# Kernel tuning notes

Measured on AMD Instinct MI355X. Metric: run time of the kernel, lower is better.

The kernel has to match this reference:

```python
import jax, jax.numpy as jnp
import numpy as np

B, N, D = 2, 2048, 1024          # batch, seq (= wh*ww), model dim
H, HD = 16, 64                   # heads, head_dim (inner_dim = H*HD = D)
MLP = 4096                       # SwiGLU hidden dim
WSY, WSX = 16, 32                # ws_y = wh//2, ws_x = ww//2  (wh=32, ww=64)
EPS = float(jnp.finfo(jnp.float32).eps)  # torch RMSNorm default eps


def setup_inputs() -> dict:
    key = jax.random.key(0)
    ks = jax.random.split(key, 8)
    return {
        "x": jax.random.normal(ks[0], (B, N, D), jnp.float32),
        "t": jax.random.normal(ks[1], (B,), jnp.float32),
        "dt": jax.random.normal(ks[2], (B, D), jnp.float32),
        "w_qkv": (jax.random.normal(ks[3], (3 * H * HD, D), jnp.float32) * 0.02),
        "w_o": (jax.random.normal(ks[4], (D, H * HD), jnp.float32) * 0.02),
        "w1": (jax.random.normal(ks[5], (2 * MLP, D), jnp.float32) * 0.02),
        "w2": (jax.random.normal(ks[6], (D, MLP), jnp.float32) * 0.02),
        "g_attn": jnp.ones((D,), jnp.float32),  # RMSNorm weight (attn)
        "g_ff": jnp.ones((D,), jnp.float32),    # RMSNorm weight (ffn)
    }


def _rms(x, g):
    return x * jax.lax.rsqrt(jnp.mean(x * x, axis=-1, keepdims=True) + EPS) * g


def _win(x):
    # 'b h (wc_y wc_x ws_y ws_x) d' -> 'b h (wc_y ws_y wc_x ws_x) d'
    b, h, n, d = x.shape
    return x.reshape(b, h, 2, 2, WSY, WSX, d).transpose(0, 1, 2, 4, 3, 5, 6).reshape(b, h, n, d)


def _unwin(x):
    # inverse of _win
    b, h, n, d = x.shape
    return x.reshape(b, h, 2, WSY, 2, WSX, d).transpose(0, 1, 2, 4, 3, 5, 6).reshape(b, h, n, d)


def reference(x, t, dt, w_qkv, w_o, w1, w2, g_attn, g_ff):
    # ---- SPAttention (pre-norm); all-to-all is identity on 1 device ----
    h = _rms(x, g_attn)
    qkv = h @ w_qkv.T                              # [B,N,3*H*HD]
    q, k, v = jnp.split(qkv, 3, axis=-1)
    as_heads = lambda z: z.reshape(B, N, H, HD).transpose(0, 2, 1, 3)  # b h n d
    q, k, v = _win(as_heads(q)), _win(as_heads(k)), _win(as_heads(v))
    # NOTE: the source computes RoPE2D(q), RoPE2D(k) but discards the result;
    # attention consumes the UNROTATED seq_gathered_q/k/v. Faithful: no rotation.
    scale = 1.0 / jnp.sqrt(jnp.float32(HD))        # SDPA default scale
    s = jnp.einsum('bhqd,bhkd->bhqk', q, k) * scale
    a = jax.nn.softmax(s, axis=-1)
    o = jnp.einsum('bhqk,bhkd->bhqd', a, v)
    o = _unwin(o).transpose(0, 2, 1, 3).reshape(B, N, H * HD)
    x = x + o @ w_o.T                               # residual
    # ---- SwiGLU FeedForward (pre-norm) + residual ----
    hf = _rms(x, g_ff)
    gate, up = jnp.split(hf @ w1.T, 2, axis=-1)
    return x + (jax.nn.silu(gate) * up) @ w2.T
```

## Files before the change

### kernel.cpp

```cpp
#include <hip/hip_runtime.h>
#include <cstdint>
#include <cstddef>

typedef __attribute__((ext_vector_type(8)))  __bf16 bf16x8;
typedef __attribute__((ext_vector_type(4)))  __bf16 bf16x4;
typedef __attribute__((ext_vector_type(4)))  float  f32x4;
typedef __attribute__((ext_vector_type(16))) float  f32x16;
typedef __attribute__((ext_vector_type(2)))  uint32_t u32x2;
typedef __attribute__((ext_vector_type(4)))  uint32_t u32x4;

#define MFMA_BF16(a, b, c) __builtin_amdgcn_mfma_f32_16x16x32_bf16((a), (b), (c), 0, 0, 0)
#define MFMA32(a, b, c)    __builtin_amdgcn_mfma_f32_32x32x16_bf16((a), (b), (c), 0, 0, 0)

__device__ __forceinline__ void gload_lds16(const __bf16* src, __bf16* lds_dst) {
    __builtin_amdgcn_global_load_lds(
        (const __attribute__((address_space(1))) void*)(const_cast<__bf16*>(src)),
        (__attribute__((address_space(3))) void*)(lds_dst), 16, 0, 0);
}

__device__ __forceinline__ uint32_t pack2(float a, float b) {
    uint16_t ua = __builtin_bit_cast(uint16_t, (__bf16)a);
    uint16_t ub = __builtin_bit_cast(uint16_t, (__bf16)b);
    return (uint32_t)ua | ((uint32_t)ub << 16);
}

__device__ __forceinline__ bf16x8 ldv(const void* p) {
    return *reinterpret_cast<const bf16x8*>(p);
}

__global__ __launch_bounds__(256) void cvt_kernel(const float* __restrict__ src,
                                                  __bf16* __restrict__ dst) {
    int i = blockIdx.x * 256 + threadIdx.x;
    float4 v = reinterpret_cast<const float4*>(src)[i];
    bf16x4 o;
    o[0] = (__bf16)v.x; o[1] = (__bf16)v.y; o[2] = (__bf16)v.z; o[3] = (__bf16)v.w;
    reinterpret_cast<bf16x4*>(dst)[i] = o;
}

__global__ __launch_bounds__(256) void rmsnorm_kernel(const float* __restrict__ x,
                                                      const float* __restrict__ g,
                                                      __bf16* __restrict__ out) {
    const int row = blockIdx.x;
    const int t = threadIdx.x;
    float4 v = reinterpret_cast<const float4*>(x + (size_t)row * 1024)[t];
    float ss = v.x * v.x + v.y * v.y + v.z * v.z + v.w * v.w;
#pragma unroll
    for (int m = 1; m < 64; m <<= 1) ss += __shfl_xor(ss, m);
    __shared__ float sred[4];
    if ((t & 63) == 0) sred[t >> 6] = ss;
    __syncthreads();
    float tot = sred[0] + sred[1] + sred[2] + sred[3];
    float rs = rsqrtf(tot * (1.0f / 1024.0f) + 1.1920928955078125e-07f);
    float4 gv = reinterpret_cast<const float4*>(g)[t];
    bf16x4 o;
    o[0] = (__bf16)(v.x * rs * gv.x);
    o[1] = (__bf16)(v.y * rs * gv.y);
    o[2] = (__bf16)(v.z * rs * gv.z);
    o[3] = (__bf16)(v.w * rs * gv.w);
    *reinterpret_cast<bf16x4*>(out + (size_t)row * 1024 + t * 4) = o;
}

template <int MODE>
__global__ __launch_bounds__(512, 2) void gemm_8p(const __bf16* __restrict__ A, int lda,
                                                  const __bf16* __restrict__ B, int ldb,
                                                  __bf16* __restrict__ outb,
                                                  int K, int ldo) {
    __shared__ __attribute__((aligned(16))) __bf16 Sl[8][256 * 32];
    const int t = threadIdx.x;
    const int lane = t & 63;
    const int wid = t >> 6;
    const int l15 = lane & 15;
    const int g4 = lane >> 4;
    const int bm = blockIdx.x, bn = blockIdx.y;
    const int wm = (wid >> 2) * 128;
    const int wn = (wid & 3) * 64;

    const __bf16 *pa[2], *pb[2];
#pragma unroll
    for (int i = 0; i < 2; ++i) {
        int L = i * 512 + t, r = L >> 2, c = (L & 3) ^ ((r >> 1) & 3);
        pa[i] = A + (size_t)(bm * 256 + r) * lda + c * 8;
        int rb = bn * 256 + r;
        int srow = (MODE == 2) ? ((rb >> 1) + ((rb & 1) << 12)) : rb;
        pb[i] = B + (size_t)srow * ldb + c * 8;
    }
    auto stageA = [&](int slot) {
#pragma unroll
        for (int i = 0; i < 2; ++i) {
            gload_lds16(pa[i], &Sl[slot][(i * 512 + t) * 8]);
            pa[i] += 32;
        }
    };
    auto stageB = [&](int slot) {
#pragma unroll
        for (int i = 0; i < 2; ++i) {
            gload_lds16(pb[i], &Sl[slot][(i * 512 + t) * 8]);
            pb[i] += 32;
        }
    };

    int aoff[8], boff[4];
#pragma unroll
    for (int m = 0; m < 8; ++m) {
        int r = wm + m * 16 + l15;
        aoff[m] = r * 64 + ((g4 ^ ((r >> 1) & 3)) * 16);
    }
#pragma unroll
    for (int n = 0; n < 4; ++n) {
        int r = wn + n * 16 + l15;
        boff[n] = r * 64 + ((g4 ^ ((r >> 1) & 3)) * 16);
    }

    f32x4 acc[8][4] = {};
    const int NT = K >> 6;

    stageA(0); stageB(1); stageA(2); stageB(3); stageA(4); stageB(5);
    asm volatile("s_waitcnt vmcnt(4)" ::: "memory");
    __builtin_amdgcn_s_barrier();

    for (int tt = 0; tt < NT; ++tt) {
        const int q = (tt & 1) * 4, nq = q ^ 4;
        const char* Alo = (const char*)&Sl[q + 0][0];
        const char* Blo = (const char*)&Sl[q + 1][0];
        const char* Ahi = (const char*)&Sl[q + 2][0];
        const char* Bhi = (const char*)&Sl[q + 3][0];
        bf16x8 af[4], bf[4];

#pragma unroll
        for (int m = 0; m < 4; ++m) af[m] = ldv(Alo + aoff[m]);
#pragma unroll
        for (int n = 0; n < 4; ++n) bf[n] = ldv(Blo + boff[n]);
        if (tt + 1 < NT) stageA(nq + 2);
        __builtin_amdgcn_s_barrier();
        __builtin_amdgcn_s_setprio(1);
#pragma unroll
        for (int m = 0; m < 4; ++m)
#pragma unroll
            for (int n = 0; n < 4; ++n)
                acc[m][n] = MFMA_BF16(af[m], bf[n], acc[m][n]);
        __builtin_amdgcn_s_setprio(0);
        __builtin_amdgcn_s_barrier();

#pragma unroll
        for (int m = 0; m < 4; ++m) af[m] = ldv(Alo + aoff[4 + m]);
        if (tt + 1 < NT) stageB(nq + 3);
        __builtin_amdgcn_s_barrier();
        __builtin_amdgcn_s_setprio(1);
#pragma unroll
        for (int m = 0; m < 4; ++m)
#pragma unroll
            for (int n = 0; n < 4; ++n)
                acc[4 + m][n] = MFMA_BF16(af[m], bf[n], acc[4 + m][n]);
        __builtin_amdgcn_s_setprio(0);
        __builtin_amdgcn_s_barrier();

#pragma unroll
        for (int m = 0; m < 4; ++m) af[m] = ldv(Ahi + aoff[m]);
#pragma unroll
        for (int n = 0; n < 4; ++n) bf[n] = ldv(Bhi + boff[n]);
        if (tt + 2 < NT) stageA(q + 0);
        __builtin_amdgcn_s_barrier();
        __builtin_amdgcn_s_setprio(1);
#pragma unroll
        for (int m = 0; m < 4; ++m)
#pragma unroll
            for (int n = 0; n < 4; ++n)
                acc[m][n] = MFMA_BF16(af[m], bf[n], acc[m][n]);
        __builtin_amdgcn_s_setprio(0);
        __builtin_amdgcn_s_barrier();

#pragma unroll
        for (int m = 0; m < 4; ++m) af[m] = ldv(Ahi + aoff[4 + m]);
        if (tt + 2 < NT) stageB(q + 1);
        __builtin_amdgcn_s_barrier();
        __builtin_amdgcn_s_setprio(1);
#pragma unroll
        for (int m = 0; m < 4; ++m)
#pragma unroll
            for (int n = 0; n < 4; ++n)
                acc[4 + m][n] = MFMA_BF16(af[m], bf[n], acc[4 + m][n]);
        __builtin_amdgcn_s_setprio(0);
        if (tt + 2 < NT) {
            asm volatile("s_waitcnt vmcnt(4)" ::: "memory");
        } else {
            asm volatile("s_waitcnt vmcnt(0)" ::: "memory");
        }
        __builtin_amdgcn_s_barrier();
    }

    const int row0 = bm * 256 + wm + (g4 << 2);
    const int col0 = bn * 256 + wn + l15;
#pragma unroll
    for (int m = 0; m < 8; ++m)
#pragma unroll
        for (int n = 0; n < 4; ++n)
#pragma unroll
            for (int r2 = 0; r2 < 4; ++r2) {
                int row = row0 + m * 16 + r2;
                int col = col0 + n * 16;
                float v = acc[m][n][r2];
                if (MODE == 0) {
                    outb[(size_t)row * ldo + col] = (__bf16)v;
                } else {
                    float pv = __shfl_xor(v, 1);
                    if (!(l15 & 1)) {
                        float sg = v / (1.0f + __expf(-v));
                        outb[(size_t)row * ldo + (col >> 1)] = (__bf16)(sg * pv);
                    }
                }
            }
}

template <int MODE, int NB>
__global__ __launch_bounds__(256) void gemm_nt(const __bf16* __restrict__ A, int lda,
                                               const __bf16* __restrict__ B, int ldb,
                                               __bf16* __restrict__ outb,
                                               float* __restrict__ outf,
                                               const float* __restrict__ resid,
                                               int K, int ldo) {
    constexpr int BN = NB * 32;
    __shared__ __attribute__((aligned(16))) __bf16 As[128 * 64];
    __shared__ __attribute__((aligned(16))) __bf16 Bs[BN * 64];
    const int t = threadIdx.x;
    const int lane = t & 63;
    const int wid = t >> 6;
    const int bm = blockIdx.x, bn = blockIdx.y;
    const int wm = (wid >> 1) * 64, wn = (wid & 1) * (NB * 16);
    f32x4 acc[4][NB] = {};

    for (int kt = 0; kt < K; kt += 64) {
        __syncthreads();
#pragma unroll
        for (int i = 0; i < 4; ++i) {
            int L = i * 256 + t;
            int r = L >> 3, s = L & 7;
            int c = s ^ (r & 7);
            gload_lds16(A + (size_t)(bm * 128 + r) * lda + kt + c * 8, As + L * 8);
        }
#pragma unroll
        for (int i = 0; i < NB; ++i) {
            int L = i * 256 + t;
            int r = L >> 3, s = L & 7;
            int c = s ^ (r & 7);
            int rb = bn * BN + r;
            gload_lds16(B + (size_t)rb * ldb + kt + c * 8, Bs + L * 8);
        }
        __syncthreads();
#pragma unroll
        for (int ks = 0; ks < 2; ++ks) {
            bf16x8 af[4], bfr[NB];
#pragma unroll
            for (int mi = 0; mi < 4; ++mi) {
                int r = wm + mi * 16 + (lane & 15);
                int slot = (ks * 4 + (lane >> 4)) ^ (r & 7);
                af[mi] = *reinterpret_cast<const bf16x8*>(As + r * 64 + slot * 8);
            }
#pragma unroll
            for (int ni = 0; ni < NB; ++ni) {
                int r = wn + ni * 16 + (lane & 15);
                int slot = (ks * 4 + (lane >> 4)) ^ (r & 7);
                bfr[ni] = *reinterpret_cast<const bf16x8*>(Bs + r * 64 + slot * 8);
            }
#pragma unroll
            for (int mi = 0; mi < 4; ++mi)
#pragma unroll
                for (int ni = 0; ni < NB; ++ni)
                    acc[mi][ni] = MFMA_BF16(af[mi], bfr[ni], acc[mi][ni]);
        }
    }
    const int row0 = bm * 128 + wm + ((lane >> 4) << 2);
    const int col0 = bn * BN + wn + (lane & 15);
#pragma unroll
    for (int mi = 0; mi < 4; ++mi)
#pragma unroll
        for (int ni = 0; ni < NB; ++ni)
#pragma unroll
            for (int r2 = 0; r2 < 4; ++r2) {
                int row = row0 + mi * 16 + r2;
                int col = col0 + ni * 16;
                float v = acc[mi][ni][r2];
                if (MODE == 0) {
                    outb[(size_t)row * ldo + col] = (__bf16)v;
                } else {
                    size_t idx = (size_t)row * ldo + col;
                    outf[idx] = v + resid[idx];
                }
            }
}

__global__ __launch_bounds__(256) void vtrans_kernel(const __bf16* __restrict__ qkv,
                                                     __bf16* __restrict__ vt) {
    __shared__ __bf16 T[64][68];
    const int t = threadIdx.x;
    const int bh = blockIdx.y, b = bh >> 4, h = bh & 15;
    const int n0 = blockIdx.x * 64;
    const __bf16* vp = qkv + (size_t)b * 2048 * 3072 + 2048 + h * 64;
#pragma unroll
    for (int i = 0; i < 2; ++i) {
        int r = i * 32 + (t >> 3), c = t & 7;
        bf16x8 v = *reinterpret_cast<const bf16x8*>(vp + (size_t)(n0 + r) * 3072 + c * 8);
#pragma unroll
        for (int j = 0; j < 8; ++j) T[c * 8 + j][r] = v[j];
    }
    __syncthreads();
#pragma unroll
    for (int i = 0; i < 2; ++i) {
        int hd = i * 32 + (t >> 3), c = t & 7;
        bf16x8 v;
#pragma unroll
        for (int j = 0; j < 8; ++j) v[j] = T[hd][c * 8 + j];
        *reinterpret_cast<bf16x8*>(vt + ((size_t)bh * 64 + hd) * 2048 + n0 + c * 8) = v;
    }
}

__global__ __launch_bounds__(256) void attn_kernel(const __bf16* __restrict__ qkv,
                                                   const __bf16* __restrict__ vt,
                                                   __bf16* __restrict__ o) {
    __shared__ __attribute__((aligned(16))) __bf16 Ks[2][128 * 64];
    __shared__ __attribute__((aligned(16))) __bf16 Vs[2][64 * 128];
    const int t = threadIdx.x;
    const int lane = t & 63;
    const int w = t >> 6;
    const int hi = lane >> 5;
    const int l31 = lane & 31;
    const int bh = blockIdx.y;
    const int b = bh >> 4, h = bh & 15;
    const __bf16* qp = qkv + (size_t)b * 2048 * 3072 + h * 64;
    const __bf16* kp = qp + 1024;
    const __bf16* vtp = vt + (size_t)bh * 64 * 2048;
    const int q0 = blockIdx.x * 128 + w * 32;

    const float SC = 0.18033688011112042f;
    bf16x8 qf[4];
#pragma unroll
    for (int s = 0; s < 4; ++s) {
        bf16x8 raw = *reinterpret_cast<const bf16x8*>(
            qp + (size_t)(q0 + l31) * 3072 + s * 16 + hi * 8);
        bf16x8 sc;
#pragma unroll
        for (int j = 0; j < 8; ++j) sc[j] = (__bf16)((float)raw[j] * SC);
        qf[s] = sc;
    }

    f32x16 oa[2] = {};
    float m_run = -INFINITY, l_run = 0.0f;

    auto stage = [&](int buf, int kt) {
#pragma unroll
        for (int i = 0; i < 4; ++i) {
            int L = i * 256 + t;
            int r = L >> 3, s = L & 7;
            int c = s ^ (r & 7);
            gload_lds16(kp + (size_t)(kt + r) * 3072 + c * 8, &Ks[buf][L * 8]);
        }
#pragma unroll
        for (int i = 0; i < 4; ++i) {
            int L = i * 256 + t;
            int r = L >> 4, s = L & 15;
            int c = s ^ (r & 15);
            gload_lds16(vtp + (size_t)r * 2048 + kt + c * 8, &Vs[buf][L * 8]);
        }
    };
    stage(0, 0);
    __syncthreads();

    for (int kt = 0; kt < 2048; kt += 128) {
        const int buf = (kt >> 7) & 1;
        if (kt + 128 < 2048) stage(buf ^ 1, kt + 128);

#pragma unroll
        for (int h2 = 0; h2 < 2; ++h2) {
            f32x16 st[2] = {};
#pragma unroll
            for (int s = 0; s < 4; ++s) {
#pragma unroll
                for (int mb = 0; mb < 2; ++mb) {
                    int r = h2 * 64 + mb * 32 + l31;
                    int sl = (s * 2 + hi) ^ (r & 7);
                    bf16x8 kf = *reinterpret_cast<const bf16x8*>(&Ks[buf][r * 64 + sl * 8]);
                    st[mb] = MFMA32(kf, qf[s], st[mb]);
                }
            }
            float mt = -INFINITY;
#pragma unroll
            for (int mb = 0; mb < 2; ++mb)
#pragma unroll
                for (int r = 0; r < 16; ++r) mt = fmaxf(mt, st[mb][r]);
            mt = fmaxf(mt, __shfl_xor(mt, 32));
            if (__any(mt > m_run + 8.0f)) {
                float m_new = fmaxf(m_run, mt);
                float alpha = exp2f(m_run - m_new);
#pragma unroll
                for (int r = 0; r < 16; ++r) {
                    float av = __shfl(alpha, (r & 3) + 8 * (r >> 2) + 4 * hi);
                    oa[0][r] *= av;
                    oa[1][r] *= av;
                }
                l_run *= alpha;
                m_run = m_new;
            }
            float ps = 0.0f;
#pragma unroll
            for (int mb = 0; mb < 2; ++mb)
#pragma unroll
                for (int r = 0; r < 16; ++r) {
                    float p = exp2f(st[mb][r] - m_run);
                    st[mb][r] = p;
                    ps += p;
                }
            ps += __shfl_xor(ps, 32);
            l_run += ps;

            uint32_t pk[16];
#pragma unroll
            for (int mb = 0; mb < 2; ++mb)
#pragma unroll
                for (int i2 = 0; i2 < 8; ++i2)
                    pk[mb * 8 + i2] = pack2(st[mb][2 * i2], st[mb][2 * i2 + 1]);

#pragma unroll
            for (int s2 = 0; s2 < 4; ++s2) {
                const int I0 = (s2 >> 1) * 8 + (s2 & 1) * 4;
                u32x2 w02 = __builtin_amdgcn_permlane32_swap(pk[I0], pk[I0 + 2], false, false);
                u32x2 w13 = __builtin_amdgcn_permlane32_swap(pk[I0 + 1], pk[I0 + 3], false, false);
                u32x4 fv;
                fv[0] = w02[0]; fv[1] = w13[0]; fv[2] = w02[1]; fv[3] = w13[1];
                bf16x8 pa = __builtin_bit_cast(bf16x8, fv);
#pragma unroll
                for (int nb = 0; nb < 2; ++nb) {
                    int rv = nb * 32 + l31;
                    int ch = h2 * 8 + s2 * 2 + hi;
                    int sl = ch ^ (rv & 15);
                    bf16x8 vf = *reinterpret_cast<const bf16x8*>(&Vs[buf][rv * 128 + sl * 8]);
                    oa[nb] = MFMA32(pa, vf, oa[nb]);
                }
            }
        }
        __syncthreads();
    }

#pragma unroll
    for (int r = 0; r < 16; ++r) {
        int crow = (r & 3) + 8 * (r >> 2) + 4 * hi;
        float lv = __shfl(l_run, crow);
        float inv = 1.0f / lv;
        int row = q0 + crow;
        size_t base = ((size_t)b * 2048 + row) * 1024 + h * 64 + l31;
        o[base]      = (__bf16)(oa[0][r] * inv);
        o[base + 32] = (__bf16)(oa[1][r] * inv);
    }
}

extern "C" void kernel_launch(void* const* d_in, const int* in_sizes, int n_in,
                              void* d_out, int out_size, void* d_ws, size_t ws_size,
                              hipStream_t stream) {
    const float* x      = (const float*)d_in[0];
    const float* w_qkv  = (const float*)d_in[3];
    const float* w_o    = (const float*)d_in[4];
    const float* w1     = (const float*)d_in[5];
    const float* w2     = (const float*)d_in[6];
    const float* g_attn = (const float*)d_in[7];
    const float* g_ff   = (const float*)d_in[8];
    float* out = (float*)d_out;

    char* ws = (char*)d_ws;
    size_t off = 0;
    auto alloc = [&](size_t bytes) -> void* {
        void* p = ws + off;
        off += (bytes + 255) & ~(size_t)255;
        return p;
    };
    __bf16* wqkv_b = (__bf16*)alloc((size_t)3072 * 1024 * 2);
    __bf16* wo_b   = (__bf16*)alloc((size_t)1024 * 1024 * 2);
    __bf16* w1_b   = (__bf16*)alloc((size_t)8192 * 1024 * 2);
    __bf16* w2_b   = (__bf16*)alloc((size_t)1024 * 4096 * 2);
    __bf16* h_b    = (__bf16*)alloc((size_t)4096 * 1024 * 2);
    __bf16* qkv_b  = (__bf16*)alloc((size_t)4096 * 3072 * 2);
    __bf16* o_b    = (__bf16*)alloc((size_t)4096 * 1024 * 2);
    float*  x2     = (float*)alloc((size_t)4096 * 1024 * 4);
    __bf16* vt_b   = (__bf16*)alloc((size_t)32 * 64 * 2048 * 2);
    __bf16* act_b  = qkv_b;

    cvt_kernel<<<3072, 256, 0, stream>>>(w_qkv, wqkv_b);
    cvt_kernel<<<1024, 256, 0, stream>>>(w_o, wo_b);
    cvt_kernel<<<8192, 256, 0, stream>>>(w1, w1_b);
    cvt_kernel<<<4096, 256, 0, stream>>>(w2, w2_b);

    rmsnorm_kernel<<<4096, 256, 0, stream>>>(x, g_attn, h_b);
    gemm_8p<0><<<dim3(16, 12), 512, 0, stream>>>(h_b, 1024, wqkv_b, 1024,
                                                 qkv_b, 1024, 3072);
    vtrans_kernel<<<dim3(32, 32), 256, 0, stream>>>(qkv_b, vt_b);
    attn_kernel<<<dim3(16, 32), 256, 0, stream>>>(qkv_b, vt_b, o_b);
    gemm_nt<1, 2><<<dim3(32, 16), 256, 0, stream>>>(o_b, 1024, wo_b, 1024,
                                                    nullptr, x2, x, 1024, 1024);
    rmsnorm_kernel<<<4096, 256, 0, stream>>>(x2, g_ff, h_b);
    gemm_8p<2><<<dim3(16, 32), 512, 0, stream>>>(h_b, 1024, w1_b, 1024,
                                                 act_b, 1024, 4096);
    gemm_nt<1, 2><<<dim3(32, 16), 256, 0, stream>>>(act_b, 4096, w2_b, 4096,
                                                    nullptr, out, x2, 4096, 1024);
}
```

Measured before the change: 321.3 us.

## Fuse weight casts, add XCD block swizzle and MFMA priority, retile QKV GEMM

Merges the four fp32-to-bf16 weight conversion launches into one kernel that dispatches by block index. Remaps block IDs in the GEMM and attention kernels so consecutive tiles land on the same XCD, aiming for better L2 reuse. Raises wave priority around the MFMA sections with s_setprio so matrix work gets issued ahead of memory work. Switches the QKV projection from the 256x256 gemm_8p kernel to gemm_nt with 128x128 tiles, which gives more workgroups at the cost of less reuse per tile.

```diff
diff --git a/kernel.cpp b/kernel.cpp
--- a/kernel.cpp
+++ b/kernel.cpp
@@ -28,13 +28,29 @@
     return *reinterpret_cast<const bf16x8*>(p);
 }
 
-__global__ __launch_bounds__(256) void cvt_kernel(const float* __restrict__ src,
-                                                  __bf16* __restrict__ dst) {
-    int i = blockIdx.x * 256 + threadIdx.x;
-    float4 v = reinterpret_cast<const float4*>(src)[i];
+__device__ __forceinline__ int xcd_swz(int lid, int n) {
+    return (lid & 7) * (n >> 3) + (lid >> 3);
+}
+
+__global__ __launch_bounds__(256) void cvt4_kernel(const float* __restrict__ s0,
+                                                   const float* __restrict__ s1,
+                                                   const float* __restrict__ s2,
+                                                   const float* __restrict__ s3,
+                                                   __bf16* __restrict__ d0,
+                                                   __bf16* __restrict__ d1,
+                                                   __bf16* __restrict__ d2,
+                                                   __bf16* __restrict__ d3) {
+    int b = blockIdx.x;
+    const float* s; __bf16* d; int off;
+    if (b < 3072)       { s = s0; d = d0; off = b; }
+    else if (b < 4096)  { s = s1; d = d1; off = b - 3072; }
+    else if (b < 12288) { s = s2; d = d2; off = b - 4096; }
+    else                { s = s3; d = d3; off = b - 12288; }
+    int i = off * 256 + threadIdx.x;
+    float4 v = reinterpret_cast<const float4*>(s)[i];
     bf16x4 o;
     o[0] = (__bf16)v.x; o[1] = (__bf16)v.y; o[2] = (__bf16)v.z; o[3] = (__bf16)v.w;
-    reinterpret_cast<bf16x4*>(dst)[i] = o;
+    reinterpret_cast<bf16x4*>(d)[i] = o;
 }
 
 __global__ __launch_bounds__(256) void rmsnorm_kernel(const float* __restrict__ x,
@@ -71,7 +87,9 @@
     const int wid = t >> 6;
     const int l15 = lane & 15;
     const int g4 = lane >> 4;
-    const int bm = blockIdx.x, bn = blockIdx.y;
+    const int nwg = gridDim.x * gridDim.y;
+    const int sid = xcd_swz(blockIdx.x + blockIdx.y * gridDim.x, nwg);
+    const int bm = sid % gridDim.x, bn = sid / gridDim.x;
     const int wm = (wid >> 2) * 128;
     const int wn = (wid & 3) * 64;
 
@@ -224,7 +242,9 @@
     const int t = threadIdx.x;
     const int lane = t & 63;
     const int wid = t >> 6;
-    const int bm = blockIdx.x, bn = blockIdx.y;
+    const int nwg = gridDim.x * gridDim.y;
+    const int sid = xcd_swz(blockIdx.x + blockIdx.y * gridDim.x, nwg);
+    const int bm = sid % gridDim.x, bn = sid / gridDim.x;
     const int wm = (wid >> 1) * 64, wn = (wid & 1) * (NB * 16);
     f32x4 acc[4][NB] = {};
 
@@ -261,11 +281,13 @@
                 int slot = (ks * 4 + (lane >> 4)) ^ (r & 7);
                 bfr[ni] = *reinterpret_cast<const bf16x8*>(Bs + r * 64 + slot * 8);
             }
+            __builtin_amdgcn_s_setprio(1);
 #pragma unroll
             for (int mi = 0; mi < 4; ++mi)
 #pragma unroll
                 for (int ni = 0; ni < NB; ++ni)
                     acc[mi][ni] = MFMA_BF16(af[mi], bfr[ni], acc[mi][ni]);
+            __builtin_amdgcn_s_setprio(0);
         }
     }
     const int row0 = bm * 128 + wm + ((lane >> 4) << 2);
@@ -323,12 +345,15 @@
     const int w = t >> 6;
     const int hi = lane >> 5;
     const int l31 = lane & 31;
-    const int bh = blockIdx.y;
+    const int nwg = gridDim.x * gridDim.y;
+    const int sid = xcd_swz(blockIdx.x + blockIdx.y * gridDim.x, nwg);
+    const int qb = sid % gridDim.x;
+    const int bh = sid / gridDim.x;
     const int b = bh >> 4, h = bh & 15;
     const __bf16* qp = qkv + (size_t)b * 2048 * 3072 + h * 64;
     const __bf16* kp = qp + 1024;
     const __bf16* vtp = vt + (size_t)bh * 64 * 2048;
-    const int q0 = blockIdx.x * 128 + w * 32;
+    const int q0 = qb * 128 + w * 32;
 
     const float SC = 0.18033688011112042f;
     bf16x8 qf[4];
@@ -371,6 +396,7 @@
 #pragma unroll
         for (int h2 = 0; h2 < 2; ++h2) {
             f32x16 st[2] = {};
+            __builtin_amdgcn_s_setprio(1);
 #pragma unroll
             for (int s = 0; s < 4; ++s) {
 #pragma unroll
@@ -381,6 +407,7 @@
                     st[mb] = MFMA32(kf, qf[s], st[mb]);
                 }
             }
+            __builtin_amdgcn_s_setprio(0);
             float mt = -INFINITY;
 #pragma unroll
             for (int mb = 0; mb < 2; ++mb)
@@ -418,6 +445,7 @@
                 for (int i2 = 0; i2 < 8; ++i2)
                     pk[mb * 8 + i2] = pack2(st[mb][2 * i2], st[mb][2 * i2 + 1]);
 
+            __builtin_amdgcn_s_setprio(1);
 #pragma unroll
             for (int s2 = 0; s2 < 4; ++s2) {
                 const int I0 = (s2 >> 1) * 8 + (s2 & 1) * 4;
@@ -435,6 +463,7 @@
                     oa[nb] = MFMA32(pa, vf, oa[nb]);
                 }
             }
+            __builtin_amdgcn_s_setprio(0);
         }
         __syncthreads();
     }
@@ -481,14 +510,12 @@
     __bf16* vt_b   = (__bf16*)alloc((size_t)32 * 64 * 2048 * 2);
     __bf16* act_b  = qkv_b;
 
-    cvt_kernel<<<3072, 256, 0, stream>>>(w_qkv, wqkv_b);
-    cvt_kernel<<<1024, 256, 0, stream>>>(w_o, wo_b);
-    cvt_kernel<<<8192, 256, 0, stream>>>(w1, w1_b);
-    cvt_kernel<<<4096, 256, 0, stream>>>(w2, w2_b);
+    cvt4_kernel<<<16384, 256, 0, stream>>>(w_qkv, w_o, w1, w2,
+                                           wqkv_b, wo_b, w1_b, w2_b);
 
     rmsnorm_kernel<<<4096, 256, 0, stream>>>(x, g_attn, h_b);
-    gemm_8p<0><<<dim3(16, 12), 512, 0, stream>>>(h_b, 1024, wqkv_b, 1024,
-                                                 qkv_b, 1024, 3072);
+    gemm_nt<0, 4><<<dim3(32, 24), 256, 0, stream>>>(h_b, 1024, wqkv_b, 1024,
+                                                    qkv_b, nullptr, nullptr, 1024, 3072);
     vtrans_kernel<<<dim3(32, 32), 256, 0, stream>>>(qkv_b, vt_b);
     attn_kernel<<<dim3(16, 32), 256, 0, stream>>>(qkv_b, vt_b, o_b);
     gemm_nt<1, 2><<<dim3(32, 16), 256, 0, stream>>>(o_b, 1024, wo_b, 1024,
```

New measurement: 313.7 us. -2.4%, faster.
